# Kernel tuning notes

Measured on AMD Instinct MI355X. Metric: run time of the kernel, lower is better.

Reference implementation:

```python
import jax, jax.numpy as jnp
import numpy as np

S, LC = 8192, 16
CE = CH = 64      # char embed == char hidden (original quirk)
WE, HW = 128, 256 # word embed, word hidden
WV, CV, TAGS = 50000, 128, 50


def _lstm_step(h, c, x, Wih, Whh, bih, bhh):
    # PyTorch LSTM gate order: i, f, g, o
    g = x @ Wih.T + h @ Whh.T + bih + bhh
    i, f, gg, o = jnp.split(g, 4, axis=-1)
    c = jax.nn.sigmoid(f) * c + jax.nn.sigmoid(i) * jnp.tanh(gg)
    h = jax.nn.sigmoid(o) * jnp.tanh(c)
    return h, c


def setup_inputs() -> dict:
    key = jax.random.key(0)
    ks = jax.random.split(key, 16)
    inp = {
        'word_idxs': jax.random.randint(ks[0], (S,), 0, WV),
        'char_idxs': jax.random.randint(ks[1], (S, LC), 0, CV),
        'char_lens': jax.random.randint(ks[2], (S,), 1, LC + 1),
        'char_emb': jax.random.normal(ks[3], (CV, CE), jnp.float32) * 0.1,
        'char_Wih': jax.random.normal(ks[4], (4 * CH, CE), jnp.float32) * 0.1,
        'char_Whh': jax.random.normal(ks[5], (4 * CH, CH), jnp.float32) * 0.1,
        'char_bih': jax.random.normal(ks[6], (4 * CH,), jnp.float32) * 0.1,
        'char_bhh': jax.random.normal(ks[7], (4 * CH,), jnp.float32) * 0.1,
        'word_emb': jax.random.normal(ks[8], (WV, WE), jnp.float32) * 0.1,
        'word_Wih': jax.random.normal(ks[9], (4 * HW, WE + CH), jnp.float32) * 0.1,
        'word_Whh': jax.random.normal(ks[10], (4 * HW, HW), jnp.float32) * 0.1,
        'word_bih': jax.random.normal(ks[11], (4 * HW,), jnp.float32) * 0.1,
        'word_bhh': jax.random.normal(ks[12], (4 * HW,), jnp.float32) * 0.1,
        'tag_W': jax.random.normal(ks[13], (TAGS, HW), jnp.float32) * 0.1,
        'tag_b': jax.random.normal(ks[14], (TAGS,), jnp.float32) * 0.1,
    }
    return inp


def reference(word_idxs, char_idxs, char_lens,
              char_emb, char_Wih, char_Whh, char_bih, char_bhh,
              word_emb, word_Wih, word_Whh, word_bih, word_bhh,
              tag_W, tag_b):
    # --- char LSTM over all words in parallel (one fused scan over char time) ---
    cx = char_emb[char_idxs]                      # [S, LC, CE]
    cx = jnp.transpose(cx, (1, 0, 2))             # [LC, S, CE]

    def cstep(carry, x_t):
        h, c = carry
        h, c = _lstm_step(h, c, x_t, char_Wih, char_Whh, char_bih, char_bhh)
        return (h, c), h

    h0 = jnp.zeros((S, CH), cx.dtype)
    (_, _), hs = jax.lax.scan(cstep, (h0, h0), cx)  # hs: [LC, S, CH]
    # original takes char_lstm_out[-1] == hidden at position len(chars)-1
    char_feat = hs[char_lens - 1, jnp.arange(S)]    # [S, CH]

    # --- word LSTM over the sentence (batch = 1) ---
    wx = jnp.concatenate([word_emb[word_idxs], char_feat], axis=-1)  # [S, WE+CH]

    def wstep(carry, x_t):
        h, c = carry
        h, c = _lstm_step(h, c, x_t, word_Wih, word_Whh, word_bih, word_bhh)
        return (h, c), h

    wh0 = jnp.zeros((HW,), wx.dtype)
    (_, _), outs = jax.lax.scan(wstep, (wh0, wh0), wx)  # [S, HW]

    logits = outs @ tag_W.T + tag_b                     # [S, TAGS]
    return jax.nn.log_softmax(logits, axis=-1)
```

## Files before the change

### kernel.cpp

```cpp
#include <hip/hip_runtime.h>
#include <hip/hip_bf16.h>

#define S_LEN 8192
#define LC 16
#define CE 64
#define CH 64
#define WE 128
#define NTAGS 50

using bf16 = __hip_bfloat16;
typedef unsigned int u32;
typedef unsigned long long u64;

__device__ __forceinline__ float bfbits2f(unsigned short u) {
    union { unsigned int i; float f; } v; v.i = ((unsigned int)u) << 16; return v.f;
}
__device__ __forceinline__ float sigm(float x) {
    return __builtin_amdgcn_rcpf(1.0f + __expf(-x));
}
__device__ __forceinline__ float tanh_fast(float x) {
    return 1.0f - 2.0f * __builtin_amdgcn_rcpf(__expf(2.0f * x) + 1.0f);
}

template <bool BF>
__device__ __forceinline__ float ld1(const void* p, size_t i) {
    if constexpr (BF) return bfbits2f(((const unsigned short*)p)[i]);
    else              return ((const float*)p)[i];
}
template <bool BF>
__device__ __forceinline__ float4 ld4(const void* p, size_t i) {
    if constexpr (BF) {
        const ushort4 s = *reinterpret_cast<const ushort4*>((const unsigned short*)p + i);
        return make_float4(bfbits2f(s.x), bfbits2f(s.y), bfbits2f(s.z), bfbits2f(s.w));
    } else {
        return *reinterpret_cast<const float4*>((const float*)p + i);
    }
}
template <bool BF>
__device__ __forceinline__ void st1(void* p, size_t i, float v) {
    if constexpr (BF) ((bf16*)p)[i] = __float2bfloat16(v);
    else              ((float*)p)[i] = v;
}

__global__ void kdetect(const void* emb, u32* flag) {
    const int j = threadIdx.x;
    int s = 0;
    #pragma unroll
    for (int k = 0; k < 4; ++k) {
        const unsigned short u = ((const unsigned short*)emb)[j * 4 + k];
        const int e = (u >> 7) & 0xFF;
        s += (e >= 100 && e <= 133) ? 1 : 0;
    }
    #pragma unroll
    for (int off = 32; off >= 1; off >>= 1) s += __shfl_xor(s, off, 64);
    if (j == 0) *flag = (s >= 200) ? 1u : 0u;
}

template <bool BF>
__global__ __launch_bounds__(256, 2) void kchar(
        const u32* __restrict__ dtf,
        const int* __restrict__ char_idxs, const int* __restrict__ char_lens,
        const void* __restrict__ char_emb,
        const void* __restrict__ Wih, const void* __restrict__ Whh,
        const void* __restrict__ bih, const void* __restrict__ bhh,
        float* __restrict__ cfeat) {
    if ((*dtf != 0u) != BF) return;
    const int j = threadIdx.x;
    const int w0 = blockIdx.x * 8;

    __shared__ __align__(16) float emb_lds[128 * CE];
    __shared__ __align__(16) float gates_lds[8 * 256];
    __shared__ __align__(16) float h_lds[8 * CH];
    __shared__ __align__(16) float c_lds[8 * CH];
    __shared__ int cidx_lds[8 * LC];
    __shared__ int len_lds[8];

    {
        float4* emb4 = reinterpret_cast<float4*>(emb_lds);
        #pragma unroll
        for (int i = 0; i < 8; ++i) {
            const int c = i * 256 + j;
            emb4[c] = ld4<BF>(char_emb, (size_t)c * 4);
        }
    }
    if (j < 128) cidx_lds[j] = char_idxs[w0 * LC + j];
    if (j < 8)   len_lds[j]  = char_lens[w0 + j];
    h_lds[j] = 0.f; h_lds[j + 256] = 0.f;
    c_lds[j] = 0.f; c_lds[j + 256] = 0.f;

    float4 wih4[16], whh4[16];
    #pragma unroll
    for (int kc = 0; kc < 16; ++kc) {
        wih4[kc] = ld4<BF>(Wih, (size_t)j * CE + kc * 4);
        whh4[kc] = ld4<BF>(Whh, (size_t)j * CH + kc * 4);
    }
    const float bias = ld1<BF>(bih, j) + ld1<BF>(bhh, j);
    __syncthreads();

    for (int t = 0; t < LC; ++t) {
        for (int w = 0; w < 8; ++w) {
            const int ci = cidx_lds[w * LC + t];
            const float4* x4  = reinterpret_cast<const float4*>(emb_lds + ci * CE);
            const float4* hh4 = reinterpret_cast<const float4*>(h_lds + w * CH);
            float a0 = 0.f, a1 = 0.f, a2 = 0.f, a3 = 0.f;
            #pragma unroll
            for (int kc = 0; kc < 16; ++kc) {
                const float4 xv = x4[kc]; const float4 hv = hh4[kc];
                const float4 wi = wih4[kc]; const float4 wh = whh4[kc];
                a0 = fmaf(wi.x, xv.x, a0); a1 = fmaf(wi.y, xv.y, a1);
                a2 = fmaf(wi.z, xv.z, a2); a3 = fmaf(wi.w, xv.w, a3);
                a0 = fmaf(wh.x, hv.x, a0); a1 = fmaf(wh.y, hv.y, a1);
                a2 = fmaf(wh.z, hv.z, a2); a3 = fmaf(wh.w, hv.w, a3);
            }
            gates_lds[w * 256 + j] = bias + ((a0 + a1) + (a2 + a3));
        }
        __syncthreads();
        #pragma unroll
        for (int rep = 0; rep < 2; ++rep) {
            const int p = j + rep * 256;
            const int w = p >> 6, u = p & 63;
            const float ig = gates_lds[w * 256 + u];
            const float fg = gates_lds[w * 256 + 64 + u];
            const float gg = gates_lds[w * 256 + 128 + u];
            const float og = gates_lds[w * 256 + 192 + u];
            const float cn = sigm(fg) * c_lds[p] + sigm(ig) * tanh_fast(gg);
            const float hn = sigm(og) * tanh_fast(cn);
            c_lds[p] = cn; h_lds[p] = hn;
            if (t == len_lds[w] - 1)
                cfeat[(size_t)(w0 + w) * CH + u] = hn;
        }
        __syncthreads();
    }
}

template <bool BF>
__global__ __launch_bounds__(256) void kgx(
        const u32* __restrict__ dtf,
        int t0, const int* __restrict__ word_idxs, const float* __restrict__ cfeat,
        const void* __restrict__ wemb, const void* __restrict__ Wih,
        const void* __restrict__ bih, const void* __restrict__ bhh,
        float* __restrict__ Gxr) {
    if ((*dtf != 0u) != BF) return;
    const int j = threadIdx.x;
    const int wr0 = blockIdx.x * 16;
    const int w0g = t0 + wr0;
    __shared__ __align__(16) float wx[16 * 192];
    __shared__ int widx[16];
    if (j < 16) widx[j] = word_idxs[w0g + j];
    __syncthreads();
    {
        const int w = j >> 4, ch = j & 15;
        const size_t eb = (size_t)widx[w] * WE + ch * 8;
        const float4 f0 = ld4<BF>(wemb, eb), f1 = ld4<BF>(wemb, eb + 4);
        float4* dst = reinterpret_cast<float4*>(wx + w * 192 + ch * 8);
        dst[0] = f0; dst[1] = f1;
        const float4 cf = *reinterpret_cast<const float4*>(
            cfeat + (size_t)(w0g + w) * CH + ch * 4);
        *reinterpret_cast<float4*>(wx + w * 192 + WE + ch * 4) = cf;
    }
    __syncthreads();

    for (int g = 0; g < 4; ++g) {
        const int r = g * 256 + j;
        float acc[16];
        #pragma unroll
        for (int w = 0; w < 16; ++w) acc[w] = 0.f;
        #pragma unroll 8
        for (int kc = 0; kc < 48; ++kc) {
            const float4 wv = ld4<BF>(Wih, (size_t)r * 192 + kc * 4);
            #pragma unroll
            for (int w = 0; w < 16; ++w) {
                const float4 xv = *reinterpret_cast<const float4*>(wx + w * 192 + kc * 4);
                acc[w] = fmaf(wv.x, xv.x, acc[w]);
                acc[w] = fmaf(wv.y, xv.y, acc[w]);
                acc[w] = fmaf(wv.z, xv.z, acc[w]);
                acc[w] = fmaf(wv.w, xv.w, acc[w]);
            }
        }
        const float bias = ld1<BF>(bih, r) + ld1<BF>(bhh, r);
        #pragma unroll
        for (int w = 0; w < 16; ++w)
            Gxr[(size_t)(wr0 + w) * 1024 + r] = acc[w] + bias;
    }
}

template <bool BF>
__global__ __launch_bounds__(1024, 4) void kwlstm(
        const u32* __restrict__ dtf,
        int t0, int t1, int epoch, const void* __restrict__ whh,
        const float* __restrict__ Gxr,
        float* __restrict__ hallr, u64* hgx2, float* csave, u32* xccpub) {
    if ((*dtf != 0u) != BF) return;
    const int j = threadIdx.x;

    __shared__ int role_s;
    const u32 etag = 0xB0u + ((u32)epoch & 0xFu);
    if (j == 0) {
        const u32 xcc = __builtin_amdgcn_s_getreg(6164) & 0xFu;
        __hip_atomic_store(&xccpub[blockIdx.x], (etag << 24) | xcc,
                           __ATOMIC_RELAXED, __HIP_MEMORY_SCOPE_AGENT);
    }
    if (j < 64) {
        u32 v;
        do {
            v = __hip_atomic_load(&xccpub[j], __ATOMIC_RELAXED,
                                  __HIP_MEMORY_SCOPE_AGENT);
        } while ((v >> 24) != etag);
        const u32 v0 = __shfl(v, 0, 64);
        const u64 mask = __ballot((v & 0xFu) == (v0 & 0xFu));
        const int myb = blockIdx.x;
        int role = -1;
        if (__popcll(mask) >= 4) {
            if ((mask >> myb) & 1ull) {
                const int rank = __popcll(mask & ((1ull << myb) - 1ull));
                if (rank < 4) role = rank;
            }
        } else {
            if (myb < 4) role = myb;
        }
        if (j == 0) role_s = role;
    }
    __syncthreads();
    const int b = role_s;
    if (b < 0) return;

    const int r  = j & 255;
    const int kq = j >> 8;
    const int R  = ((r >> 6) << 8) + b * 64 + (r & 63);

    __shared__ __align__(16) float h_cur[256];
    __shared__ __align__(16) float part[1024];

    float4 wv[16];
    #pragma unroll
    for (int kc = 0; kc < 16; ++kc)
        wv[kc] = ld4<BF>(whh, (size_t)R * 256 + kq * 64 + kc * 4);

    if (j < 256) h_cur[j] = 0.f;
    float c_reg = 0.f;
    if (t0 > 0 && j < 64) c_reg = csave[b * 64 + j];

    float gxA = (j < 256) ? Gxr[(size_t)0 * 1024 + R] : 0.f;
    float gxB = (j < 256 && t0 + 1 < t1) ? Gxr[(size_t)1 * 1024 + R] : 0.f;
    __syncthreads();

    for (int t = t0; t < t1; ++t) {
        if (t > 0) {
            if (t == t0) {
                if (j < 256) {
                    u64 pk;
                    do {
                        pk = __hip_atomic_load(&hgx2[(size_t)(t & 1) * 256 + j],
                                               __ATOMIC_RELAXED, __HIP_MEMORY_SCOPE_AGENT);
                    } while ((u32)(pk >> 32) != (u32)t);
                    h_cur[j] = __uint_as_float((u32)pk);
                }
            } else {
                if (j < 192) {
                    const int gu = j + (j >= b * 64 ? 64 : 0);
                    u64 pk;
                    do {
                        pk = __hip_atomic_load(&hgx2[(size_t)(t & 1) * 256 + gu],
                                               __ATOMIC_RELAXED, __HIP_MEMORY_SCOPE_AGENT);
                    } while ((u32)(pk >> 32) != (u32)t);
                    h_cur[gu] = __uint_as_float((u32)pk);
                }
            }
        }
        __syncthreads();
        float gxN = 0.f;
        if (j < 256 && t + 2 < t1)
            gxN = Gxr[(size_t)(t + 2 - t0) * 1024 + R];
        float a0 = 0.f, a1 = 0.f, a2 = 0.f, a3 = 0.f;
        const float4* h4 = reinterpret_cast<const float4*>(h_cur) + kq * 16;
        #pragma unroll
        for (int kc = 0; kc < 16; ++kc) {
            const float4 hv = h4[kc];
            a0 = fmaf(wv[kc].x, hv.x, a0);
            a1 = fmaf(wv[kc].y, hv.y, a1);
            a2 = fmaf(wv[kc].z, hv.z, a2);
            a3 = fmaf(wv[kc].w, hv.w, a3);
        }
        part[j] = ((a0 + a1) + (a2 + a3)) + (kq == 0 ? gxA : 0.f);
        __syncthreads();
        if (j < 64) {
            const float ig = part[j]       + part[j + 256] + part[j + 512] + part[j + 768];
            const float fg = part[j + 64]  + part[j + 320] + part[j + 576] + part[j + 832];
            const float gg = part[j + 128] + part[j + 384] + part[j + 640] + part[j + 896];
            const float og = part[j + 192] + part[j + 448] + part[j + 704] + part[j + 960];
            const float cn = sigm(fg) * c_reg + sigm(ig) * tanh_fast(gg);
            c_reg = cn;
            const float hn = sigm(og) * tanh_fast(cn);
            const u64 pk = ((u64)(u32)(t + 1) << 32) | (u64)__float_as_uint(hn);
            __hip_atomic_store(&hgx2[(size_t)((t + 1) & 1) * 256 + b * 64 + j], pk,
                               __ATOMIC_RELAXED, __HIP_MEMORY_SCOPE_AGENT);
            h_cur[b * 64 + j] = hn;
            hallr[(size_t)(t - t0) * 256 + b * 64 + j] = hn;
        }
        gxA = gxB; gxB = gxN;
    }
    if (j < 64) csave[b * 64 + j] = c_reg;
}

template <bool BF>
__global__ __launch_bounds__(64) void ktag(
        const u32* __restrict__ dtf,
        int t0, const float* __restrict__ hallr, const void* __restrict__ tagW,
        const void* __restrict__ tagb, void* __restrict__ out) {
    if ((*dtf != 0u) != BF) return;
    const int tr = blockIdx.x, j = threadIdx.x;
    const int t = t0 + tr;
    __shared__ __align__(16) float4 h4[64];
    h4[j] = reinterpret_cast<const float4*>(hallr + (size_t)tr * 256)[j];
    __syncthreads();
    float logit = -1e30f;
    if (j < NTAGS) {
        float a0 = 0.f, a1 = 0.f, a2 = 0.f, a3 = 0.f;
        #pragma unroll
        for (int kc = 0; kc < 64; ++kc) {
            const float4 wvv = ld4<BF>(tagW, (size_t)j * 256 + kc * 4);
            const float4 hv = h4[kc];
            a0 = fmaf(wvv.x, hv.x, a0); a1 = fmaf(wvv.y, hv.y, a1);
            a2 = fmaf(wvv.z, hv.z, a2); a3 = fmaf(wvv.w, hv.w, a3);
        }
        logit = ld1<BF>(tagb, j) + ((a0 + a1) + (a2 + a3));
    }
    float m = logit;
    #pragma unroll
    for (int off = 32; off >= 1; off >>= 1) m = fmaxf(m, __shfl_xor(m, off, 64));
    const float e = (j < NTAGS) ? __expf(logit - m) : 0.f;
    float ssum = e;
    #pragma unroll
    for (int off = 32; off >= 1; off >>= 1) ssum += __shfl_xor(ssum, off, 64);
    if (j < NTAGS)
        st1<BF>(out, (size_t)t * NTAGS + j, logit - m - __logf(ssum));
}

extern "C" void kernel_launch(void* const* d_in, const int* in_sizes, int n_in,
                              void* d_out, int out_size, void* d_ws, size_t ws_size,
                              hipStream_t stream) {
    const int*  word_idxs = (const int*)d_in[0];
    const int*  char_idxs = (const int*)d_in[1];
    const int*  char_lens = (const int*)d_in[2];
    const void* char_emb  = d_in[3];
    const void* char_Wih  = d_in[4];
    const void* char_Whh  = d_in[5];
    const void* char_bih  = d_in[6];
    const void* char_bhh  = d_in[7];
    const void* word_emb  = d_in[8];
    const void* word_Wih  = d_in[9];
    const void* word_Whh  = d_in[10];
    const void* word_bih  = d_in[11];
    const void* word_bhh  = d_in[12];
    const void* tag_W     = d_in[13];
    const void* tag_b     = d_in[14];

    char* ws = (char*)d_ws;
    u32*   dtf    = (u32*)(ws);
    u64*   hgx2   = (u64*)(ws + 64);
    float* csave  = (float*)(ws + 4224);
    u32*   xccpub = (u32*)(ws + 5248);
    float* cfeat  = (float*)(ws + 8192);
    const size_t ring0 = 8192 + (size_t)S_LEN * CH * 4;

    int NC = 256;
    const int ncs[9] = {1, 2, 4, 8, 16, 32, 64, 128, 256};
    for (int i = 0; i < 9; ++i) {
        const int ct = S_LEN / ncs[i];
        if (ring0 + (size_t)ct * 5120 <= ws_size) { NC = ncs[i]; break; }
    }
    const int CT = S_LEN / NC;
    float* Gxr   = (float*)(ws + ring0);
    float* hallr = (float*)(ws + ring0 + (size_t)CT * 4096);

    hipLaunchKernelGGL(kdetect, dim3(1), dim3(64), 0, stream, char_emb, dtf);
    hipLaunchKernelGGL(kchar<true>,  dim3(S_LEN / 8), dim3(256), 0, stream,
                       dtf, char_idxs, char_lens, char_emb, char_Wih, char_Whh,
                       char_bih, char_bhh, cfeat);
    hipLaunchKernelGGL(kchar<false>, dim3(S_LEN / 8), dim3(256), 0, stream,
                       dtf, char_idxs, char_lens, char_emb, char_Wih, char_Whh,
                       char_bih, char_bhh, cfeat);
    for (int c = 0; c < NC; ++c) {
        const int t0 = c * CT;
        hipLaunchKernelGGL(kgx<true>,  dim3(CT / 16), dim3(256), 0, stream,
                           dtf, t0, word_idxs, cfeat, word_emb, word_Wih,
                           word_bih, word_bhh, Gxr);
        hipLaunchKernelGGL(kgx<false>, dim3(CT / 16), dim3(256), 0, stream,
                           dtf, t0, word_idxs, cfeat, word_emb, word_Wih,
                           word_bih, word_bhh, Gxr);
        hipLaunchKernelGGL(kwlstm<true>,  dim3(64), dim3(1024), 0, stream,
                           dtf, t0, t0 + CT, c, word_Whh, Gxr, hallr, hgx2, csave, xccpub);
        hipLaunchKernelGGL(kwlstm<false>, dim3(64), dim3(1024), 0, stream,
                           dtf, t0, t0 + CT, c, word_Whh, Gxr, hallr, hgx2, csave, xccpub);
        hipLaunchKernelGGL(ktag<true>,  dim3(CT), dim3(64), 0, stream,
                           dtf, t0, hallr, tag_W, tag_b, d_out);
        hipLaunchKernelGGL(ktag<false>, dim3(CT), dim3(64), 0, stream,
                           dtf, t0, hallr, tag_W, tag_b, d_out);
    }
}
```

Baseline: 14.13 ms.

## Use fp16 dot2 for word LSTM recurrence, halve block, add L2 polling path

```diff
diff --git a/kernel.cpp b/kernel.cpp
--- a/kernel.cpp
+++ b/kernel.cpp
@@ -1,5 +1,6 @@
 #include <hip/hip_runtime.h>
 #include <hip/hip_bf16.h>
+#include <hip/hip_fp16.h>
 
 #define S_LEN 8192
 #define LC 16
@@ -40,6 +41,55 @@
 __device__ __forceinline__ void st1(void* p, size_t i, float v) {
     if constexpr (BF) ((bf16*)p)[i] = __float2bfloat16(v);
     else              ((float*)p)[i] = v;
+}
+
+typedef _Float16 h2t __attribute__((ext_vector_type(2)));
+
+__device__ __forceinline__ u32 pk2(float a, float b) {
+    __half2 h = __floats2half2_rn(a, b);
+    u32 r; __builtin_memcpy(&r, &h, 4); return r;
+}
+__device__ __forceinline__ float fdot2u(u32 a, u32 b, float c) {
+#if __has_builtin(__builtin_amdgcn_fdot2)
+    h2t av, bv;
+    __builtin_memcpy(&av, &a, 4);
+    __builtin_memcpy(&bv, &b, 4);
+    return __builtin_amdgcn_fdot2(av, bv, c, false);
+#else
+    __half2 ah, bh;
+    __builtin_memcpy(&ah, &a, 4);
+    __builtin_memcpy(&bh, &b, 4);
+    c = fmaf(__half2float(ah.x), __half2float(bh.x), c);
+    c = fmaf(__half2float(ah.y), __half2float(bh.y), c);
+    return c;
+#endif
+}
+
+__device__ __forceinline__ u64 ld_l2(const u64* p) {
+    u64 v;
+    asm volatile("global_load_dwordx2 %0, %1, off sc0\n\t"
+                 "s_waitcnt vmcnt(0)"
+                 : "=&v"(v) : "v"(p) : "memory");
+    return v;
+}
+__device__ __forceinline__ void st_l2(u64* p, u64 v) {
+    asm volatile("global_store_dwordx2 %0, %1, off sc0"
+                 :: "v"(p), "v"(v) : "memory");
+}
+__device__ __forceinline__ u64 poll_pkt(u64* p, u32 want, bool& fastb) {
+    u64 pk;
+    if (fastb) {
+        int guard = 0;
+        for (;;) {
+            pk = ld_l2(p);
+            if ((u32)(pk >> 32) == want) return pk;
+            if (++guard > (1 << 15)) { fastb = false; break; }
+        }
+    }
+    do {
+        pk = __hip_atomic_load(p, __ATOMIC_RELAXED, __HIP_MEMORY_SCOPE_AGENT);
+    } while ((u32)(pk >> 32) != want);
+    return pk;
 }
 
 __global__ void kdetect(const void* emb, u32* flag) {
@@ -185,7 +235,7 @@
 }
 
 template <bool BF>
-__global__ __launch_bounds__(1024, 4) void kwlstm(
+__global__ __launch_bounds__(512, 2) void kwlstm(
         const u32* __restrict__ dtf,
         int t0, int t1, int epoch, const void* __restrict__ whh,
         const float* __restrict__ Gxr,
@@ -194,6 +244,7 @@
     const int j = threadIdx.x;
 
     __shared__ int role_s;
+    __shared__ int fast_s;
     const u32 etag = 0xB0u + ((u32)epoch & 0xFu);
     if (j == 0) {
         const u32 xcc = __builtin_amdgcn_s_getreg(6164) & 0xFu;
@@ -209,8 +260,9 @@
         const u32 v0 = __shfl(v, 0, 64);
         const u64 mask = __ballot((v & 0xFu) == (v0 & 0xFu));
         const int myb = blockIdx.x;
-        int role = -1;
+        int role = -1, fast = 0;
         if (__popcll(mask) >= 4) {
+            fast = 1;
             if ((mask >> myb) & 1ull) {
                 const int rank = __popcll(mask & ((1ull << myb) - 1ull));
                 if (rank < 4) role = rank;
@@ -218,25 +270,29 @@
         } else {
             if (myb < 4) role = myb;
         }
-        if (j == 0) role_s = role;
+        if (j == 0) { role_s = role; fast_s = fast; }
     }
     __syncthreads();
     const int b = role_s;
     if (b < 0) return;
+    bool fastb = (fast_s != 0);
 
     const int r  = j & 255;
     const int kq = j >> 8;
     const int R  = ((r >> 6) << 8) + b * 64 + (r & 63);
 
-    __shared__ __align__(16) float h_cur[256];
-    __shared__ __align__(16) float part[1024];
-
-    float4 wv[16];
-    #pragma unroll
-    for (int kc = 0; kc < 16; ++kc)
-        wv[kc] = ld4<BF>(whh, (size_t)R * 256 + kq * 64 + kc * 4);
-
-    if (j < 256) h_cur[j] = 0.f;
+    __shared__ __align__(16) u32  h2[128];
+    __shared__ __align__(16) float part[512];
+
+    u32 wv2[64];
+    #pragma unroll
+    for (int kc = 0; kc < 32; ++kc) {
+        const float4 w = ld4<BF>(whh, (size_t)R * 256 + kq * 128 + kc * 4);
+        wv2[2 * kc]     = pk2(w.x, w.y);
+        wv2[2 * kc + 1] = pk2(w.z, w.w);
+    }
+
+    if (j < 128) h2[j] = 0u;
     float c_reg = 0.f;
     if (t0 > 0 && j < 64) c_reg = csave[b * 64 + j];
 
@@ -248,22 +304,20 @@
         if (t > 0) {
             if (t == t0) {
                 if (j < 256) {
-                    u64 pk;
-                    do {
-                        pk = __hip_atomic_load(&hgx2[(size_t)(t & 1) * 256 + j],
-                                               __ATOMIC_RELAXED, __HIP_MEMORY_SCOPE_AGENT);
-                    } while ((u32)(pk >> 32) != (u32)t);
-                    h_cur[j] = __uint_as_float((u32)pk);
+                    const u64 pk = poll_pkt(&hgx2[(size_t)(t & 1) * 256 + j],
+                                            (u32)t, fastb);
+                    const float hv = __uint_as_float((u32)pk);
+                    const float ho = __shfl_xor(hv, 1, 64);
+                    if (!(j & 1)) h2[j >> 1] = pk2(hv, ho);
                 }
             } else {
                 if (j < 192) {
                     const int gu = j + (j >= b * 64 ? 64 : 0);
-                    u64 pk;
-                    do {
-                        pk = __hip_atomic_load(&hgx2[(size_t)(t & 1) * 256 + gu],
-                                               __ATOMIC_RELAXED, __HIP_MEMORY_SCOPE_AGENT);
-                    } while ((u32)(pk >> 32) != (u32)t);
-                    h_cur[gu] = __uint_as_float((u32)pk);
+                    const u64 pk = poll_pkt(&hgx2[(size_t)(t & 1) * 256 + gu],
+                                            (u32)t, fastb);
+                    const float hv = __uint_as_float((u32)pk);
+                    const float ho = __shfl_xor(hv, 1, 64);
+                    if (!(j & 1)) h2[gu >> 1] = pk2(hv, ho);
                 }
             }
         }
@@ -272,29 +326,32 @@
         if (j < 256 && t + 2 < t1)
             gxN = Gxr[(size_t)(t + 2 - t0) * 1024 + R];
         float a0 = 0.f, a1 = 0.f, a2 = 0.f, a3 = 0.f;
-        const float4* h4 = reinterpret_cast<const float4*>(h_cur) + kq * 16;
+        const uint4* h4 = reinterpret_cast<const uint4*>(h2 + kq * 64);
         #pragma unroll
         for (int kc = 0; kc < 16; ++kc) {
-            const float4 hv = h4[kc];
-            a0 = fmaf(wv[kc].x, hv.x, a0);
-            a1 = fmaf(wv[kc].y, hv.y, a1);
-            a2 = fmaf(wv[kc].z, hv.z, a2);
-            a3 = fmaf(wv[kc].w, hv.w, a3);
+            const uint4 hv = h4[kc];
+            a0 = fdot2u(wv2[4 * kc + 0], hv.x, a0);
+            a1 = fdot2u(wv2[4 * kc + 1], hv.y, a1);
+            a2 = fdot2u(wv2[4 * kc + 2], hv.z, a2);
+            a3 = fdot2u(wv2[4 * kc + 3], hv.w, a3);
         }
         part[j] = ((a0 + a1) + (a2 + a3)) + (kq == 0 ? gxA : 0.f);
         __syncthreads();
         if (j < 64) {
-            const float ig = part[j]       + part[j + 256] + part[j + 512] + part[j + 768];
-            const float fg = part[j + 64]  + part[j + 320] + part[j + 576] + part[j + 832];
-            const float gg = part[j + 128] + part[j + 384] + part[j + 640] + part[j + 896];
-            const float og = part[j + 192] + part[j + 448] + part[j + 704] + part[j + 960];
+            const float ig = part[j]       + part[j + 256];
+            const float fg = part[j + 64]  + part[j + 320];
+            const float gg = part[j + 128] + part[j + 384];
+            const float og = part[j + 192] + part[j + 448];
             const float cn = sigm(fg) * c_reg + sigm(ig) * tanh_fast(gg);
             c_reg = cn;
             const float hn = sigm(og) * tanh_fast(cn);
             const u64 pk = ((u64)(u32)(t + 1) << 32) | (u64)__float_as_uint(hn);
-            __hip_atomic_store(&hgx2[(size_t)((t + 1) & 1) * 256 + b * 64 + j], pk,
-                               __ATOMIC_RELAXED, __HIP_MEMORY_SCOPE_AGENT);
-            h_cur[b * 64 + j] = hn;
+            u64* pp = &hgx2[(size_t)((t + 1) & 1) * 256 + b * 64 + j];
+            if (fastb) st_l2(pp, pk);
+            __hip_atomic_store(pp, pk, __ATOMIC_RELAXED,
+                               __HIP_MEMORY_SCOPE_AGENT);
+            const float ho = __shfl_xor(hn, 1, 64);
+            if (!(j & 1)) h2[(b * 64 + j) >> 1] = pk2(hn, ho);
             hallr[(size_t)(t - t0) * 256 + b * 64 + j] = hn;
         }
         gxA = gxB; gxB = gxN;
@@ -388,9 +445,9 @@
         hipLaunchKernelGGL(kgx<false>, dim3(CT / 16), dim3(256), 0, stream,
                            dtf, t0, word_idxs, cfeat, word_emb, word_Wih,
                            word_bih, word_bhh, Gxr);
-        hipLaunchKernelGGL(kwlstm<true>,  dim3(64), dim3(1024), 0, stream,
+        hipLaunchKernelGGL(kwlstm<true>,  dim3(64), dim3(512), 0, stream,
                            dtf, t0, t0 + CT, c, word_Whh, Gxr, hallr, hgx2, csave, xccpub);
-        hipLaunchKernelGGL(kwlstm<false>, dim3(64), dim3(1024), 0, stream,
+        hipLaunchKernelGGL(kwlstm<false>, dim3(64), dim3(512), 0, stream,
                            dtf, t0, t0 + CT, c, word_Whh, Gxr, hallr, hgx2, csave, xccpub);
         hipLaunchKernelGGL(ktag<true>,  dim3(CT), dim3(64), 0, stream,
                            dtf, t0, hallr, tag_W, tag_b, d_out);
```

Measured after the change: 27.34 ms. 93.6% more time.
